# Optimization experiments

Measured on AMD Instinct MI355X. Metric: run time of the kernel, lower is better.

The kernel has to match this reference:

```python
import jax, jax.numpy as jnp
import numpy as np

P, F, V = 2048, 8192, 2048


def setup_inputs() -> dict:
    key = jax.random.key(0)
    k1, k2, k3 = jax.random.split(key, 3)
    points = jax.random.normal(k1, (P, 3), dtype=jnp.float32)
    vertices = jax.random.normal(k2, (V, 3), dtype=jnp.float32)
    faces = jax.random.randint(k3, (F, 3), 0, V, dtype=jnp.int32)
    return {"points": points, "vertices": vertices, "faces": faces}


def _triangle_weights(points, a, b, c):
    """Barycentric weights of closest point on each triangle (a,b,c) [F,3]
    for each point [P,3], via Ericson's region classification.
    All pairwise dot products expanded so only [P,F] scalars are materialized
    (never [P,F,3] differences)."""
    ab = b - a  # [F,3]
    ac = c - a  # [F,3]
    pab = points @ ab.T  # [P,F] = dot(p, ab)
    pac = points @ ac.T  # [P,F] = dot(p, ac)
    d1 = pab - jnp.sum(a * ab, -1)  # dot(ab, p-a)
    d2 = pac - jnp.sum(a * ac, -1)  # dot(ac, p-a)
    d3 = pab - jnp.sum(b * ab, -1)  # dot(ab, p-b)
    d4 = pac - jnp.sum(b * ac, -1)  # dot(ac, p-b)
    d5 = pab - jnp.sum(c * ab, -1)  # dot(ab, p-c)
    d6 = pac - jnp.sum(c * ac, -1)  # dot(ac, p-c)
    vc = d1 * d4 - d3 * d2
    vb = d5 * d2 - d1 * d6
    va = d3 * d6 - d5 * d4

    def sdiv(n, d):
        ds = jnp.where(d == 0, 1.0, d)
        return n / ds

    # region 7 (interior) is the default; overwrite with higher-priority
    denom = va + vb + vc
    v7 = sdiv(vb, denom)
    w7 = sdiv(vc, denom)
    w1, w2, w3 = 1.0 - v7 - w7, v7, w7
    # region 6: edge bc
    t6 = sdiv(d4 - d3, (d4 - d3) + (d5 - d6))
    m6 = (va <= 0) & (d4 - d3 >= 0) & (d5 - d6 >= 0)
    w1 = jnp.where(m6, 0.0, w1)
    w2 = jnp.where(m6, 1.0 - t6, w2)
    w3 = jnp.where(m6, t6, w3)
    # region 5: edge ac
    t5 = sdiv(d2, d2 - d6)
    m5 = (vb <= 0) & (d2 >= 0) & (d6 <= 0)
    w1 = jnp.where(m5, 1.0 - t5, w1)
    w2 = jnp.where(m5, 0.0, w2)
    w3 = jnp.where(m5, t5, w3)
    # region 4: vertex c
    m4 = (d6 >= 0) & (d5 <= d6)
    w1 = jnp.where(m4, 0.0, w1)
    w2 = jnp.where(m4, 0.0, w2)
    w3 = jnp.where(m4, 1.0, w3)
    # region 3: edge ab
    t3 = sdiv(d1, d1 - d3)
    m3 = (vc <= 0) & (d1 >= 0) & (d3 <= 0)
    w1 = jnp.where(m3, 1.0 - t3, w1)
    w2 = jnp.where(m3, t3, w2)
    w3 = jnp.where(m3, 0.0, w3)
    # region 2: vertex b
    m2 = (d3 >= 0) & (d4 <= d3)
    w1 = jnp.where(m2, 0.0, w1)
    w2 = jnp.where(m2, 1.0, w2)
    w3 = jnp.where(m2, 0.0, w3)
    # region 1: vertex a
    m1 = (d1 <= 0) & (d2 <= 0)
    w1 = jnp.where(m1, 1.0, w1)
    w2 = jnp.where(m1, 0.0, w2)
    w3 = jnp.where(m1, 0.0, w3)
    return w1, w2, w3  # each [P,F]


def reference(points, vertices, faces):
    # gather per-face vertex triples (the f1/f2/f3 of the torch module)
    a = vertices[faces[:, 0]]  # [F,3]
    b = vertices[faces[:, 1]]
    c = vertices[faces[:, 2]]
    w1, w2, w3 = _triangle_weights(points, a, b, c)  # [P,F] each
    cp = w1[..., None] * a + w2[..., None] * b + w3[..., None] * c  # [P,F,3]
    dist = jnp.sum((points[:, None, :] - cp) ** 2, axis=-1)  # [P,F]
    idx = jnp.argmin(dist, axis=1)  # [P] closest face per point
    gather = lambda w: jnp.take_along_axis(w, idx[:, None], axis=1)[:, 0]
    return idx, gather(w1), gather(w2), gather(w3)
```

## Files before the change

kernel.cpp:

```cpp
#include <hip/hip_runtime.h>
#include <cstdint>

#pragma clang fp contract(off)

typedef float v2f __attribute__((ext_vector_type(2)));

#define P_N 2048
#define F_N 8192
#define V_N 2048

#define TPB 256
#define FACES_PER_TILE 32

__device__ __forceinline__ void face_setup(
    const float* __restrict__ vertices, const int* __restrict__ faces, int f,
    float* fd)
{
#pragma clang fp contract(off)
    int i0 = faces[3 * f + 0];
    int i1 = faces[3 * f + 1];
    int i2 = faces[3 * f + 2];
    float ax = vertices[3 * i0 + 0], ay = vertices[3 * i0 + 1], az = vertices[3 * i0 + 2];
    float bx = vertices[3 * i1 + 0], by = vertices[3 * i1 + 1], bz = vertices[3 * i1 + 2];
    float cx = vertices[3 * i2 + 0], cy = vertices[3 * i2 + 1], cz = vertices[3 * i2 + 2];
    float abx = bx - ax, aby = by - ay, abz = bz - az;
    float acx = cx - ax, acy = cy - ay, acz = cz - az;
    float daab = (ax * abx + ay * aby) + az * abz;
    float daac = (ax * acx + ay * acy) + az * acz;
    float dbab = (bx * abx + by * aby) + bz * abz;
    float dbac = (bx * acx + by * acy) + bz * acz;
    float dcab = (cx * abx + cy * aby) + cz * abz;
    float dcac = (cx * acx + cy * acy) + cz * acz;
    fd[0] = ax;  fd[1] = ay;  fd[2] = az;
    fd[3] = bx;  fd[4] = by;  fd[5] = bz;
    fd[6] = cx;  fd[7] = cy;  fd[8] = cz;
    fd[9] = abx; fd[10] = aby; fd[11] = abz;
    fd[12] = acx; fd[13] = acy; fd[14] = acz;
    fd[15] = daab; fd[16] = daac; fd[17] = dbab;
    fd[18] = dbac; fd[19] = dcab; fd[20] = dcac;
}

__device__ __forceinline__ void region_w(
    float d1, float d2, float d3, float d4, float d5, float d6,
    float va, float vb, float vc, float e63, float e65, float denom,
    float& w1, float& w2, float& w3)
{
#pragma clang fp contract(off)
    bool m1 = (d1 <= 0.0f) & (d2 <= 0.0f);
    bool m2 = (d3 >= 0.0f) & (d4 <= d3);
    bool m3 = (vc <= 0.0f) & (d1 >= 0.0f) & (d3 <= 0.0f);
    bool m4 = (d6 >= 0.0f) & (d5 <= d6);
    bool m5 = (vb <= 0.0f) & (d2 >= 0.0f) & (d6 <= 0.0f);
    bool m6 = (va <= 0.0f) & (e63 >= 0.0f) & (e65 >= 0.0f);
    bool anym = m1 | m2 | m3 | m4 | m5 | m6;

    float n1  = m1 ? 0.0f : m2 ? 0.0f : m3 ? d1          : m4 ? 0.0f : m5 ? d2          : m6 ? e63         : vb;
    float ds1 = m1 ? 1.0f : m2 ? 1.0f : m3 ? (d1 - d3)   : m4 ? 1.0f : m5 ? (d2 - d6)   : m6 ? (e63 + e65) : denom;
    ds1 = (ds1 == 0.0f) ? 1.0f : ds1;
    float n2  = anym ? 0.0f : vc;
    float ds2 = anym ? 1.0f : ((denom == 0.0f) ? 1.0f : denom);

    float q1 = n1 / ds1;
    float q2 = n2 / ds2;
    float u = (1.0f - q1) - q2;

    w1 = m1 ? 1.0f : m2 ? 0.0f : m3 ? u    : m4 ? 0.0f : m5 ? u    : m6 ? 0.0f : u;
    w2 = m1 ? 0.0f : m2 ? 1.0f : m3 ? q1   : m4 ? 0.0f : m5 ? 0.0f : m6 ? u    : q1;
    w3 = m1 ? 0.0f : m2 ? 0.0f : m3 ? 0.0f : m4 ? 1.0f : m5 ? q1   : m6 ? q1   : q2;
}

__device__ __forceinline__ void tri_eval_exact(
    float px, float py, float pz,
    const float* fd,
    float& w1o, float& w2o, float& w3o, float& disto)
{
#pragma clang fp contract(off)
    const float ax = fd[0], ay = fd[1], az = fd[2];
    const float bx = fd[3], by = fd[4], bz = fd[5];
    const float cx = fd[6], cy = fd[7], cz = fd[8];
    const float abx = fd[9], aby = fd[10], abz = fd[11];
    const float acx = fd[12], acy = fd[13], acz = fd[14];
    const float daab = fd[15], daac = fd[16], dbab = fd[17];
    const float dbac = fd[18], dcab = fd[19], dcac = fd[20];

    float pab = fmaf(pz, abz, fmaf(py, aby, px * abx));
    float pac = fmaf(pz, acz, fmaf(py, acy, px * acx));

    float d1 = pab - daab;
    float d2 = pac - daac;
    float d3 = pab - dbab;
    float d4 = pac - dbac;
    float d5 = pab - dcab;
    float d6 = pac - dcac;

    float vc = d1 * d4 - d3 * d2;
    float vb = d5 * d2 - d1 * d6;
    float va = d3 * d6 - d5 * d4;

    float denom = (va + vb) + vc;
    float dn = (denom == 0.0f) ? 1.0f : denom;
    float v7 = vb / dn;
    float w7 = vc / dn;
    float w1 = (1.0f - v7) - w7;
    float w2 = v7;
    float w3 = w7;

    float e63 = d4 - d3;
    float e65 = d5 - d6;
    float t6d = e63 + e65; t6d = (t6d == 0.0f) ? 1.0f : t6d;
    float t6 = e63 / t6d;
    if ((va <= 0.0f) & (e63 >= 0.0f) & (e65 >= 0.0f)) { w1 = 0.0f; w2 = 1.0f - t6; w3 = t6; }

    float t5d = d2 - d6; t5d = (t5d == 0.0f) ? 1.0f : t5d;
    float t5 = d2 / t5d;
    if ((vb <= 0.0f) & (d2 >= 0.0f) & (d6 <= 0.0f)) { w1 = 1.0f - t5; w2 = 0.0f; w3 = t5; }

    if ((d6 >= 0.0f) & (d5 <= d6)) { w1 = 0.0f; w2 = 0.0f; w3 = 1.0f; }

    float t3d = d1 - d3; t3d = (t3d == 0.0f) ? 1.0f : t3d;
    float t3 = d1 / t3d;
    if ((vc <= 0.0f) & (d1 >= 0.0f) & (d3 <= 0.0f)) { w1 = 1.0f - t3; w2 = t3; w3 = 0.0f; }

    if ((d3 >= 0.0f) & (d4 <= d3)) { w1 = 0.0f; w2 = 1.0f; w3 = 0.0f; }

    if ((d1 <= 0.0f) & (d2 <= 0.0f)) { w1 = 1.0f; w2 = 0.0f; w3 = 0.0f; }

    float cpx = (w1 * ax + w2 * bx) + w3 * cx;
    float cpy = (w1 * ay + w2 * by) + w3 * cy;
    float cpz = (w1 * az + w2 * bz) + w3 * cz;
    float dx = px - cpx, dy = py - cpy, dz = pz - cpz;
    float dist = (dx * dx + dy * dy) + dz * dz;

    w1o = w1; w2o = w2; w3o = w3; disto = dist;
}

__global__ __launch_bounds__(TPB) void k_scan(
    const float* __restrict__ points,
    const float* __restrict__ vertices,
    const int* __restrict__ faces,
    unsigned long long* __restrict__ best)
{
#pragma clang fp contract(off)
    __shared__ float sq[21][FACES_PER_TILE];

    const int pblk = blockIdx.x;
    const int fblk = blockIdx.y;
    const int t = threadIdx.x;

    if (t < FACES_PER_TILE) {
        int f = fblk * FACES_PER_TILE + t;
        float fd[21];
        face_setup(vertices, faces, f, fd);
#pragma unroll
        for (int k = 0; k < 21; ++k) sq[k][t] = fd[k];
    }
    __syncthreads();

    const int p = pblk * TPB + t;
    const float px = points[3 * p + 0];
    const float py = points[3 * p + 1];
    const float pz = points[3 * p + 2];
    const v2f pxv = {px, px};
    const v2f pyv = {py, py};
    const v2f pzv = {pz, pz};

    unsigned int bestdb = 0xffffffffu;
    int bestf = 0;
    const int fbase = fblk * FACES_PER_TILE;

#pragma unroll 2
    for (int j = 0; j < FACES_PER_TILE; j += 2) {
#define LD2(q) (*(const v2f*)&sq[q][j])
        v2f axv = LD2(0),  ayv = LD2(1),  azv = LD2(2);
        v2f bxv = LD2(3),  byv = LD2(4),  bzv = LD2(5);
        v2f cxv = LD2(6),  cyv = LD2(7),  czv = LD2(8);
        v2f abxv = LD2(9),  abyv = LD2(10), abzv = LD2(11);
        v2f acxv = LD2(12), acyv = LD2(13), aczv = LD2(14);
        v2f daabv = LD2(15), daacv = LD2(16), dbabv = LD2(17);
        v2f dbacv = LD2(18), dcabv = LD2(19), dcacv = LD2(20);
#undef LD2

        v2f pab = __builtin_elementwise_fma(pzv, abzv,
                    __builtin_elementwise_fma(pyv, abyv, pxv * abxv));
        v2f pac = __builtin_elementwise_fma(pzv, aczv,
                    __builtin_elementwise_fma(pyv, acyv, pxv * acxv));

        v2f d1 = pab - daabv;
        v2f d2 = pac - daacv;
        v2f d3 = pab - dbabv;
        v2f d4 = pac - dbacv;
        v2f d5 = pab - dcabv;
        v2f d6 = pac - dcacv;

        v2f vcv = d1 * d4 - d3 * d2;
        v2f vbv = d5 * d2 - d1 * d6;
        v2f vav = d3 * d6 - d5 * d4;

        v2f e63 = d4 - d3;
        v2f e65 = d5 - d6;
        v2f denom = (vav + vbv) + vcv;

        float w1a, w2a, w3a, w1b, w2b, w3b;
        region_w(d1.x, d2.x, d3.x, d4.x, d5.x, d6.x,
                 vav.x, vbv.x, vcv.x, e63.x, e65.x, denom.x, w1a, w2a, w3a);
        region_w(d1.y, d2.y, d3.y, d4.y, d5.y, d6.y,
                 vav.y, vbv.y, vcv.y, e63.y, e65.y, denom.y, w1b, w2b, w3b);

        v2f w1v = {w1a, w1b};
        v2f w2v = {w2a, w2b};
        v2f w3v = {w3a, w3b};

        v2f cpx = (w1v * axv + w2v * bxv) + w3v * cxv;
        v2f cpy = (w1v * ayv + w2v * byv) + w3v * cyv;
        v2f cpz = (w1v * azv + w2v * bzv) + w3v * czv;
        v2f dx = pxv - cpx, dy = pyv - cpy, dz = pzv - cpz;
        v2f dist = (dx * dx + dy * dy) + dz * dz;

        float da = dist.x;
        float db = dist.y;
        unsigned int ua = __float_as_uint(da);
        unsigned int ub = __float_as_uint(db);
        if (da != da) ua = 0u;
        if (db != db) ub = 0u;
        if (ua < bestdb) { bestdb = ua; bestf = fbase + j; }
        if (ub < bestdb) { bestdb = ub; bestf = fbase + j + 1; }
    }

    unsigned long long key =
        ((unsigned long long)bestdb << 32) | (unsigned int)bestf;
    atomicMin(&best[p], key);
}

__global__ __launch_bounds__(TPB) void k_final(
    const float* __restrict__ points,
    const float* __restrict__ vertices,
    const int* __restrict__ faces,
    const unsigned long long* __restrict__ best,
    float* __restrict__ out)
{
    const int p = blockIdx.x * TPB + threadIdx.x;
    if (p >= P_N) return;
    unsigned long long bk = best[p];
    int f = (int)(bk & 0xffffffffull);

    float fd[21];
    face_setup(vertices, faces, f, fd);

    const float px = points[3 * p + 0];
    const float py = points[3 * p + 1];
    const float pz = points[3 * p + 2];
    float w1, w2, w3, dist;
    tri_eval_exact(px, py, pz, fd, w1, w2, w3, dist);

    out[p] = (float)f;
    out[P_N + p] = w1;
    out[2 * P_N + p] = w2;
    out[3 * P_N + p] = w3;
}

extern "C" void kernel_launch(void* const* d_in, const int* in_sizes, int n_in,
                              void* d_out, int out_size, void* d_ws, size_t ws_size,
                              hipStream_t stream)
{
    const float* points = (const float*)d_in[0];
    const float* vertices = (const float*)d_in[1];
    const int* faces = (const int*)d_in[2];
    float* out = (float*)d_out;
    unsigned long long* best = (unsigned long long*)d_ws;

    hipMemsetAsync(d_ws, 0xFF, P_N * sizeof(unsigned long long), stream);

    dim3 grid(P_N / TPB, F_N / FACES_PER_TILE);
    k_scan<<<grid, TPB, 0, stream>>>(points, vertices, faces, best);
    k_final<<<(P_N + TPB - 1) / TPB, TPB, 0, stream>>>(points, vertices, faces, best, out);
}
```

Baseline: 55.95 us.

## Add bound-screening pass so exact evaluation runs only for candidate faces

Splits the brute-force scan into two passes. A screening kernel computes cheap per-face lower and upper distance bounds for each point, stores 16-bit truncated lower bounds in a workspace buffer and atomically reduces the minimum upper bound. An exact kernel then runs the full triangle evaluation only for faces whose lower bound does not exceed that minimum. The aim is to skip most exact evaluations, at the cost of an extra launch, a large lower-bound buffer (about 32 MB written and reread), divergent branches, and reliance on hand-tuned numeric margins for correctness. If the workspace is too small it falls back to the old full scan.

```diff
diff --git a/kernel.cpp b/kernel.cpp
--- a/kernel.cpp
+++ b/kernel.cpp
@@ -7,10 +7,15 @@
 
 #define P_N 2048
 #define F_N 8192
-#define V_N 2048
-
 #define TPB 256
-#define FACES_PER_TILE 32
+#define FPT 32
+#define NT (F_N / FPT)
+
+#define WS_BEST_OFF   0
+#define WS_MINUB_OFF  16384
+#define WS_LB_OFF     24576
+#define WS_NEEDED     (24576ull + (unsigned long long)(F_N / 2) * P_N * 4ull)
+
 
 __device__ __forceinline__ void face_setup(
     const float* __restrict__ vertices, const int* __restrict__ faces, int f,
@@ -40,6 +45,307 @@
     fd[18] = dbac; fd[19] = dcab; fd[20] = dcac;
 }
 
+__device__ __forceinline__ void tri_eval_exact(
+    float px, float py, float pz,
+    const float* fd,
+    float& w1o, float& w2o, float& w3o, float& disto)
+{
+#pragma clang fp contract(off)
+    const float ax = fd[0], ay = fd[1], az = fd[2];
+    const float bx = fd[3], by = fd[4], bz = fd[5];
+    const float cx = fd[6], cy = fd[7], cz = fd[8];
+    const float abx = fd[9], aby = fd[10], abz = fd[11];
+    const float acx = fd[12], acy = fd[13], acz = fd[14];
+    const float daab = fd[15], daac = fd[16], dbab = fd[17];
+    const float dbac = fd[18], dcab = fd[19], dcac = fd[20];
+
+    float pab = fmaf(pz, abz, fmaf(py, aby, px * abx));
+    float pac = fmaf(pz, acz, fmaf(py, acy, px * acx));
+
+    float d1 = pab - daab;
+    float d2 = pac - daac;
+    float d3 = pab - dbab;
+    float d4 = pac - dbac;
+    float d5 = pab - dcab;
+    float d6 = pac - dcac;
+
+    float vc = d1 * d4 - d3 * d2;
+    float vb = d5 * d2 - d1 * d6;
+    float va = d3 * d6 - d5 * d4;
+
+    float denom = (va + vb) + vc;
+    float dn = (denom == 0.0f) ? 1.0f : denom;
+    float v7 = vb / dn;
+    float w7 = vc / dn;
+    float w1 = (1.0f - v7) - w7;
+    float w2 = v7;
+    float w3 = w7;
+
+    float e63 = d4 - d3;
+    float e65 = d5 - d6;
+    float t6d = e63 + e65; t6d = (t6d == 0.0f) ? 1.0f : t6d;
+    float t6 = e63 / t6d;
+    if ((va <= 0.0f) & (e63 >= 0.0f) & (e65 >= 0.0f)) { w1 = 0.0f; w2 = 1.0f - t6; w3 = t6; }
+
+    float t5d = d2 - d6; t5d = (t5d == 0.0f) ? 1.0f : t5d;
+    float t5 = d2 / t5d;
+    if ((vb <= 0.0f) & (d2 >= 0.0f) & (d6 <= 0.0f)) { w1 = 1.0f - t5; w2 = 0.0f; w3 = t5; }
+
+    if ((d6 >= 0.0f) & (d5 <= d6)) { w1 = 0.0f; w2 = 0.0f; w3 = 1.0f; }
+
+    float t3d = d1 - d3; t3d = (t3d == 0.0f) ? 1.0f : t3d;
+    float t3 = d1 / t3d;
+    if ((vc <= 0.0f) & (d1 >= 0.0f) & (d3 <= 0.0f)) { w1 = 1.0f - t3; w2 = t3; w3 = 0.0f; }
+
+    if ((d3 >= 0.0f) & (d4 <= d3)) { w1 = 0.0f; w2 = 1.0f; w3 = 0.0f; }
+
+    if ((d1 <= 0.0f) & (d2 <= 0.0f)) { w1 = 1.0f; w2 = 0.0f; w3 = 0.0f; }
+
+    float cpx = (w1 * ax + w2 * bx) + w3 * cx;
+    float cpy = (w1 * ay + w2 * by) + w3 * cy;
+    float cpz = (w1 * az + w2 * bz) + w3 * cz;
+    float dx = px - cpx, dy = py - cpy, dz = pz - cpz;
+    float dist = (dx * dx + dy * dy) + dz * dz;
+
+    w1o = w1; w2o = w2; w3o = w3; disto = dist;
+}
+
+
+#define NARR 35
+enum {
+    iAX = 0, iAY, iAZ,
+    iABX, iABY, iABZ,
+    iACX, iACY, iACZ,
+    iA, iB, iC, iD, iE, iF,
+    iKCS, iKCT, iKCC,
+    iKBS, iKBT, iKBC,
+    iKAS, iKAT, iKAC,
+    iNX, iNY, iNZ, iMND,
+    iIAB, iIAC, iIBC, iINN,
+    iABAB, iACAC,
+    iMARG
+};
+
+__device__ __forceinline__ void stage_screen(
+    const float* __restrict__ v, const int* __restrict__ fc, int f, int slot,
+    float sq[NARR][FPT])
+{
+#pragma clang fp contract(off)
+    int i0 = fc[3 * f + 0], i1 = fc[3 * f + 1], i2 = fc[3 * f + 2];
+    float ax = v[3 * i0], ay = v[3 * i0 + 1], az = v[3 * i0 + 2];
+    float bx = v[3 * i1], by = v[3 * i1 + 1], bz = v[3 * i1 + 2];
+    float cx = v[3 * i2], cy = v[3 * i2 + 1], cz = v[3 * i2 + 2];
+    float abx = bx - ax, aby = by - ay, abz = bz - az;
+    float acx = cx - ax, acy = cy - ay, acz = cz - az;
+    float A = (ax * abx + ay * aby) + az * abz;
+    float B = (ax * acx + ay * acy) + az * acz;
+    float C = (bx * abx + by * aby) + bz * abz;
+    float D = (bx * acx + by * acy) + bz * acz;
+    float E = (cx * abx + cy * aby) + cz * abz;
+    float F = (cx * acx + cy * acy) + cz * acz;
+    float kcs = B - D, kct = C - A, kcc = A * D - C * B;
+    float kbs = F - B, kbt = A - E, kbc = E * B - A * F;
+    float kas = D - F, kat = E - C, kac = C * F - E * D;
+    float nx = aby * acz - abz * acy;
+    float ny = abz * acx - abx * acz;
+    float nz = abx * acy - aby * acx;
+    float nn = (nx * nx + ny * ny) + nz * nz;
+    float abab = (abx * abx + aby * aby) + abz * abz;
+    float acac = (acx * acx + acy * acy) + acz * acz;
+    float bcx = cx - bx, bcy = cy - by, bcz = cz - bz;
+    float bcbc = (bcx * bcx + bcy * bcy) + bcz * bcz;
+    float inv_ab = abab > 0.0f ? 1.0f / abab : 0.0f;
+    float inv_ac = acac > 0.0f ? 1.0f / acac : 0.0f;
+    float inv_bc = bcbc > 0.0f ? 1.0f / bcbc : 0.0f;
+    float inv_nn = nn >= 1e-2f ? 1.0f / nn : 0.0f;
+    float L2 = abab + acac;
+    float infl = 1e-4f * L2 * sqrtf(L2) * inv_nn;
+    float marg = 3e-4f + infl * infl;
+    bool bad = (nn < 1e-2f) | (abab < 1e-3f) | (acac < 1e-3f) | (bcbc < 1e-3f) | (marg > 0.25f);
+    if (bad) marg = 1e30f;
+    float mnda = -((nx * ax + ny * ay) + nz * az);
+
+    sq[iAX][slot] = ax;  sq[iAY][slot] = ay;  sq[iAZ][slot] = az;
+    sq[iABX][slot] = abx; sq[iABY][slot] = aby; sq[iABZ][slot] = abz;
+    sq[iACX][slot] = acx; sq[iACY][slot] = acy; sq[iACZ][slot] = acz;
+    sq[iA][slot] = A; sq[iB][slot] = B; sq[iC][slot] = C;
+    sq[iD][slot] = D; sq[iE][slot] = E; sq[iF][slot] = F;
+    sq[iKCS][slot] = kcs; sq[iKCT][slot] = kct; sq[iKCC][slot] = kcc;
+    sq[iKBS][slot] = kbs; sq[iKBT][slot] = kbt; sq[iKBC][slot] = kbc;
+    sq[iKAS][slot] = kas; sq[iKAT][slot] = kat; sq[iKAC][slot] = kac;
+    sq[iNX][slot] = nx; sq[iNY][slot] = ny; sq[iNZ][slot] = nz; sq[iMND][slot] = mnda;
+    sq[iIAB][slot] = inv_ab; sq[iIAC][slot] = inv_ac; sq[iIBC][slot] = inv_bc; sq[iINN][slot] = inv_nn;
+    sq[iABAB][slot] = abab; sq[iACAC][slot] = acac;
+    sq[iMARG][slot] = marg;
+}
+
+__device__ __forceinline__ void screen_face(
+    float d1, float d2, float d3, float d4, float d5, float d6,
+    float va, float vb, float vc, float e63, float e65,
+    float pa2, float pb2, float pc2,
+    float sub3, float sub5, float sub6, float subI,
+    float marg,
+    float& ubmin, unsigned& lb16)
+{
+    bool m1 = (d1 <= 0.0f) & (d2 <= 0.0f);
+    bool m2 = (d3 >= 0.0f) & (d4 <= d3);
+    bool m3 = (vc <= 0.0f) & (d1 >= 0.0f) & (d3 <= 0.0f);
+    bool m4 = (d6 >= 0.0f) & (d5 <= d6);
+    bool m5 = (vb <= 0.0f) & (d2 >= 0.0f) & (d6 <= 0.0f);
+    bool m6 = (va <= 0.0f) & (e63 >= 0.0f) & (e65 >= 0.0f);
+    float screen = m1 ? pa2 : m2 ? pb2 : m3 ? sub3 : m4 ? pc2 : m5 ? sub5 : m6 ? sub6 : subI;
+    screen = fmaxf(screen, 0.0f);
+    bool bad = marg > 0.25f;
+    float ub = bad ? (pa2 + 3e-4f) : (screen + marg);
+    ubmin = fminf(ubmin, ub);
+    float lb = fmaxf(fmaf(0.99f, screen, -marg), 0.0f);
+    lb16 = __float_as_uint(lb) >> 16;
+}
+
+__global__ __launch_bounds__(TPB) void k_screen(
+    const float* __restrict__ points,
+    const float* __restrict__ vertices,
+    const int* __restrict__ faces,
+    unsigned* __restrict__ minub,
+    unsigned* __restrict__ lbout)
+{
+#pragma clang fp contract(off)
+    __shared__ float sq[NARR][FPT];
+
+    const int pblk = blockIdx.x;
+    const int fblk = blockIdx.y;
+    const int t = threadIdx.x;
+
+    if (t < FPT) stage_screen(vertices, faces, fblk * FPT + t, t, sq);
+    __syncthreads();
+
+    const int p = pblk * TPB + t;
+    const float px = points[3 * p + 0];
+    const float py = points[3 * p + 1];
+    const float pz = points[3 * p + 2];
+    const v2f pxv = {px, px}, pyv = {py, py}, pzv = {pz, pz};
+    const v2f n2v = {-2.0f, -2.0f};
+
+    float ubmin = 3e38f;
+
+#pragma unroll 2
+    for (int jp = 0; jp < FPT / 2; ++jp) {
+        const int j = jp * 2;
+#define L2D(k) (*(const v2f*)&sq[k][j])
+        v2f s = __builtin_elementwise_fma(pzv, L2D(iABZ),
+                    __builtin_elementwise_fma(pyv, L2D(iABY), pxv * L2D(iABX)));
+        v2f tt = __builtin_elementwise_fma(pzv, L2D(iACZ),
+                    __builtin_elementwise_fma(pyv, L2D(iACY), pxv * L2D(iACX)));
+
+        v2f d1 = s - L2D(iA);
+        v2f d2 = tt - L2D(iB);
+        v2f d3 = s - L2D(iC);
+        v2f d4 = tt - L2D(iD);
+        v2f d5 = s - L2D(iE);
+        v2f d6 = tt - L2D(iF);
+
+        v2f vc = __builtin_elementwise_fma(s, L2D(iKCS),
+                    __builtin_elementwise_fma(tt, L2D(iKCT), L2D(iKCC)));
+        v2f vb = __builtin_elementwise_fma(s, L2D(iKBS),
+                    __builtin_elementwise_fma(tt, L2D(iKBT), L2D(iKBC)));
+        v2f va = __builtin_elementwise_fma(s, L2D(iKAS),
+                    __builtin_elementwise_fma(tt, L2D(iKAT), L2D(iKAC)));
+
+        v2f e63 = d4 - d3;
+        v2f e65 = d5 - d6;
+
+        v2f nd = __builtin_elementwise_fma(L2D(iNZ), pzv,
+                    __builtin_elementwise_fma(L2D(iNY), pyv,
+                        __builtin_elementwise_fma(L2D(iNX), pxv, L2D(iMND))));
+
+        v2f dax = pxv - L2D(iAX);
+        v2f day = pyv - L2D(iAY);
+        v2f daz = pzv - L2D(iAZ);
+        v2f pa2 = __builtin_elementwise_fma(daz, daz,
+                     __builtin_elementwise_fma(day, day, dax * dax));
+        v2f pb2 = __builtin_elementwise_fma(n2v, d1, pa2) + L2D(iABAB);
+        v2f pc2 = __builtin_elementwise_fma(n2v, d2, pa2) + L2D(iACAC);
+
+        v2f sub3 = __builtin_elementwise_fma(-(d1 * L2D(iIAB)), d1, pa2);
+        v2f sub5 = __builtin_elementwise_fma(-(d2 * L2D(iIAC)), d2, pa2);
+        v2f sub6 = __builtin_elementwise_fma(-(e63 * L2D(iIBC)), e63, pb2);
+        v2f subI = (nd * L2D(iINN)) * nd;
+
+        v2f mg = L2D(iMARG);
+#undef L2D
+
+        unsigned lo16, hi16;
+        screen_face(d1.x, d2.x, d3.x, d4.x, d5.x, d6.x, va.x, vb.x, vc.x,
+                    e63.x, e65.x, pa2.x, pb2.x, pc2.x,
+                    sub3.x, sub5.x, sub6.x, subI.x, mg.x, ubmin, lo16);
+        screen_face(d1.y, d2.y, d3.y, d4.y, d5.y, d6.y, va.y, vb.y, vc.y,
+                    e63.y, e65.y, pa2.y, pb2.y, pc2.y,
+                    sub3.y, sub5.y, sub6.y, subI.y, mg.y, ubmin, hi16);
+
+        lbout[(fblk * (FPT / 2) + jp) * P_N + p] = lo16 | (hi16 << 16);
+    }
+
+    atomicMin(&minub[p], __float_as_uint(ubmin));
+}
+
+
+__global__ __launch_bounds__(TPB) void k_exact(
+    const float* __restrict__ points,
+    const float* __restrict__ vertices,
+    const int* __restrict__ faces,
+    const unsigned* __restrict__ minub,
+    const unsigned* __restrict__ lbin,
+    unsigned long long* __restrict__ best)
+{
+    __shared__ float sf[FPT][21];
+
+    const int pblk = blockIdx.x;
+    const int fblk = blockIdx.y;
+    const int t = threadIdx.x;
+
+    if (t < FPT) {
+        float fd[21];
+        face_setup(vertices, faces, fblk * FPT + t, fd);
+#pragma unroll
+        for (int k = 0; k < 21; ++k) sf[t][k] = fd[k];
+    }
+    __syncthreads();
+
+    const int p = pblk * TPB + t;
+    const float px = points[3 * p + 0];
+    const float py = points[3 * p + 1];
+    const float pz = points[3 * p + 2];
+    const float mub = __uint_as_float(minub[p]);
+
+    unsigned long long bk = ~0ull;
+    const int fbase = fblk * FPT;
+
+    for (int jp = 0; jp < FPT / 2; ++jp) {
+        unsigned w = lbin[(fblk * (FPT / 2) + jp) * P_N + p];
+        float lo = __uint_as_float(w << 16);
+        float hi = __uint_as_float(w & 0xFFFF0000u);
+        if (lo <= mub) {
+            float w1, w2, w3, dist;
+            tri_eval_exact(px, py, pz, &sf[jp * 2][0], w1, w2, w3, dist);
+            unsigned db = __float_as_uint(dist);
+            if (dist != dist) db = 0u;
+            unsigned long long key = ((unsigned long long)db << 32) | (unsigned)(fbase + jp * 2);
+            bk = (key < bk) ? key : bk;
+        }
+        if (hi <= mub) {
+            float w1, w2, w3, dist;
+            tri_eval_exact(px, py, pz, &sf[jp * 2 + 1][0], w1, w2, w3, dist);
+            unsigned db = __float_as_uint(dist);
+            if (dist != dist) db = 0u;
+            unsigned long long key = ((unsigned long long)db << 32) | (unsigned)(fbase + jp * 2 + 1);
+            bk = (key < bk) ? key : bk;
+        }
+    }
+
+    if (bk != ~0ull) atomicMin(&best[p], bk);
+}
+
+
 __device__ __forceinline__ void region_w(
     float d1, float d2, float d3, float d4, float d5, float d6,
     float va, float vb, float vc, float e63, float e65, float denom,
@@ -54,8 +360,8 @@
     bool m6 = (va <= 0.0f) & (e63 >= 0.0f) & (e65 >= 0.0f);
     bool anym = m1 | m2 | m3 | m4 | m5 | m6;
 
-    float n1  = m1 ? 0.0f : m2 ? 0.0f : m3 ? d1          : m4 ? 0.0f : m5 ? d2          : m6 ? e63         : vb;
-    float ds1 = m1 ? 1.0f : m2 ? 1.0f : m3 ? (d1 - d3)   : m4 ? 1.0f : m5 ? (d2 - d6)   : m6 ? (e63 + e65) : denom;
+    float n1  = m1 ? 0.0f : m2 ? 0.0f : m3 ? d1        : m4 ? 0.0f : m5 ? d2        : m6 ? e63       : vb;
+    float ds1 = m1 ? 1.0f : m2 ? 1.0f : m3 ? (d1 - d3) : m4 ? 1.0f : m5 ? (d2 - d6) : m6 ? (e63 + e65) : denom;
     ds1 = (ds1 == 0.0f) ? 1.0f : ds1;
     float n2  = anym ? 0.0f : vc;
     float ds2 = anym ? 1.0f : ((denom == 0.0f) ? 1.0f : denom);
@@ -69,86 +375,21 @@
     w3 = m1 ? 0.0f : m2 ? 0.0f : m3 ? 0.0f : m4 ? 1.0f : m5 ? q1   : m6 ? q1   : q2;
 }
 
-__device__ __forceinline__ void tri_eval_exact(
-    float px, float py, float pz,
-    const float* fd,
-    float& w1o, float& w2o, float& w3o, float& disto)
-{
-#pragma clang fp contract(off)
-    const float ax = fd[0], ay = fd[1], az = fd[2];
-    const float bx = fd[3], by = fd[4], bz = fd[5];
-    const float cx = fd[6], cy = fd[7], cz = fd[8];
-    const float abx = fd[9], aby = fd[10], abz = fd[11];
-    const float acx = fd[12], acy = fd[13], acz = fd[14];
-    const float daab = fd[15], daac = fd[16], dbab = fd[17];
-    const float dbac = fd[18], dcab = fd[19], dcac = fd[20];
-
-    float pab = fmaf(pz, abz, fmaf(py, aby, px * abx));
-    float pac = fmaf(pz, acz, fmaf(py, acy, px * acx));
-
-    float d1 = pab - daab;
-    float d2 = pac - daac;
-    float d3 = pab - dbab;
-    float d4 = pac - dbac;
-    float d5 = pab - dcab;
-    float d6 = pac - dcac;
-
-    float vc = d1 * d4 - d3 * d2;
-    float vb = d5 * d2 - d1 * d6;
-    float va = d3 * d6 - d5 * d4;
-
-    float denom = (va + vb) + vc;
-    float dn = (denom == 0.0f) ? 1.0f : denom;
-    float v7 = vb / dn;
-    float w7 = vc / dn;
-    float w1 = (1.0f - v7) - w7;
-    float w2 = v7;
-    float w3 = w7;
-
-    float e63 = d4 - d3;
-    float e65 = d5 - d6;
-    float t6d = e63 + e65; t6d = (t6d == 0.0f) ? 1.0f : t6d;
-    float t6 = e63 / t6d;
-    if ((va <= 0.0f) & (e63 >= 0.0f) & (e65 >= 0.0f)) { w1 = 0.0f; w2 = 1.0f - t6; w3 = t6; }
-
-    float t5d = d2 - d6; t5d = (t5d == 0.0f) ? 1.0f : t5d;
-    float t5 = d2 / t5d;
-    if ((vb <= 0.0f) & (d2 >= 0.0f) & (d6 <= 0.0f)) { w1 = 1.0f - t5; w2 = 0.0f; w3 = t5; }
-
-    if ((d6 >= 0.0f) & (d5 <= d6)) { w1 = 0.0f; w2 = 0.0f; w3 = 1.0f; }
-
-    float t3d = d1 - d3; t3d = (t3d == 0.0f) ? 1.0f : t3d;
-    float t3 = d1 / t3d;
-    if ((vc <= 0.0f) & (d1 >= 0.0f) & (d3 <= 0.0f)) { w1 = 1.0f - t3; w2 = t3; w3 = 0.0f; }
-
-    if ((d3 >= 0.0f) & (d4 <= d3)) { w1 = 0.0f; w2 = 1.0f; w3 = 0.0f; }
-
-    if ((d1 <= 0.0f) & (d2 <= 0.0f)) { w1 = 1.0f; w2 = 0.0f; w3 = 0.0f; }
-
-    float cpx = (w1 * ax + w2 * bx) + w3 * cx;
-    float cpy = (w1 * ay + w2 * by) + w3 * cy;
-    float cpz = (w1 * az + w2 * bz) + w3 * cz;
-    float dx = px - cpx, dy = py - cpy, dz = pz - cpz;
-    float dist = (dx * dx + dy * dy) + dz * dz;
-
-    w1o = w1; w2o = w2; w3o = w3; disto = dist;
-}
-
-__global__ __launch_bounds__(TPB) void k_scan(
+__global__ __launch_bounds__(TPB) void k_scan_full(
     const float* __restrict__ points,
     const float* __restrict__ vertices,
     const int* __restrict__ faces,
     unsigned long long* __restrict__ best)
 {
 #pragma clang fp contract(off)
-    __shared__ float sq[21][FACES_PER_TILE];
+    __shared__ float sq[21][FPT];
 
     const int pblk = blockIdx.x;
     const int fblk = blockIdx.y;
     const int t = threadIdx.x;
 
-    if (t < FACES_PER_TILE) {
-        int f = fblk * FACES_PER_TILE + t;
+    if (t < FPT) {
+        int f = fblk * FPT + t;
         float fd[21];
         face_setup(vertices, faces, f, fd);
 #pragma unroll
@@ -160,16 +401,14 @@
     const float px = points[3 * p + 0];
     const float py = points[3 * p + 1];
     const float pz = points[3 * p + 2];
-    const v2f pxv = {px, px};
-    const v2f pyv = {py, py};
-    const v2f pzv = {pz, pz};
+    const v2f pxv = {px, px}, pyv = {py, py}, pzv = {pz, pz};
 
     unsigned int bestdb = 0xffffffffu;
     int bestf = 0;
-    const int fbase = fblk * FACES_PER_TILE;
+    const int fbase = fblk * FPT;
 
 #pragma unroll 2
-    for (int j = 0; j < FACES_PER_TILE; j += 2) {
+    for (int j = 0; j < FPT; j += 2) {
 #define LD2(q) (*(const v2f*)&sq[q][j])
         v2f axv = LD2(0),  ayv = LD2(1),  azv = LD2(2);
         v2f bxv = LD2(3),  byv = LD2(4),  bzv = LD2(5);
@@ -231,6 +470,7 @@
     atomicMin(&best[p], key);
 }
 
+
 __global__ __launch_bounds__(TPB) void k_final(
     const float* __restrict__ points,
     const float* __restrict__ vertices,
@@ -266,11 +506,23 @@
     const float* vertices = (const float*)d_in[1];
     const int* faces = (const int*)d_in[2];
     float* out = (float*)d_out;
-    unsigned long long* best = (unsigned long long*)d_ws;
-
-    hipMemsetAsync(d_ws, 0xFF, P_N * sizeof(unsigned long long), stream);
-
-    dim3 grid(P_N / TPB, F_N / FACES_PER_TILE);
-    k_scan<<<grid, TPB, 0, stream>>>(points, vertices, faces, best);
+
+    char* ws = (char*)d_ws;
+    unsigned long long* best = (unsigned long long*)(ws + WS_BEST_OFF);
+
+    hipMemsetAsync(best, 0xFF, P_N * sizeof(unsigned long long), stream);
+
+    dim3 grid(P_N / TPB, NT);
+
+    if (ws_size >= WS_NEEDED) {
+        unsigned* minub = (unsigned*)(ws + WS_MINUB_OFF);
+        unsigned* lbbuf = (unsigned*)(ws + WS_LB_OFF);
+        hipMemsetAsync(minub, 0x7F, P_N * sizeof(unsigned), stream);
+        k_screen<<<grid, TPB, 0, stream>>>(points, vertices, faces, minub, lbbuf);
+        k_exact<<<grid, TPB, 0, stream>>>(points, vertices, faces, minub, lbbuf, best);
+    } else {
+        k_scan_full<<<grid, TPB, 0, stream>>>(points, vertices, faces, best);
+    }
+
     k_final<<<(P_N + TPB - 1) / TPB, TPB, 0, stream>>>(points, vertices, faces, best, out);
 }
```

New measurement: 70.59 us. +26.2%, slower.

## Add screen-then-verify path with per-face lower bounds and candidate queue

Applied to the files above, without the earlier changes.

Adds a three-kernel path: precompute an extended per-face table, run a cheap branch-light screening pass that yields 8-bit quantized lower bounds plus a per-point upper bound, then evaluate the exact Ericson routine only on faces whose bound passes the threshold. The screening pass avoids the per-face divisions of the exact scan. In exchange it writes a 16 MB byte-code array to workspace and reads it back. The margins are heuristic, so correctness depends on them, and if the workspace is too small the code falls back to the old path.

```diff
diff --git a/kernel.cpp b/kernel.cpp
--- a/kernel.cpp
+++ b/kernel.cpp
@@ -7,10 +7,17 @@
 
 #define P_N 2048
 #define F_N 8192
-#define V_N 2048
-
 #define TPB 256
-#define FACES_PER_TILE 32
+#define FPT 32
+#define NT (F_N / FPT)
+#define NC 44
+#define QCAP 192
+
+#define WS_TAB_OFF    0
+#define WS_MINUB_OFF  1441792
+#define WS_LB_OFF     2097152
+#define WS_NEEDED     (WS_LB_OFF + (size_t)P_N * F_N)
+
 
 __device__ __forceinline__ void face_setup(
     const float* __restrict__ vertices, const int* __restrict__ faces, int f,
@@ -40,6 +47,317 @@
     fd[18] = dbac; fd[19] = dcab; fd[20] = dcac;
 }
 
+__device__ __forceinline__ void tri_eval_exact(
+    float px, float py, float pz,
+    const float* fd,
+    float& w1o, float& w2o, float& w3o, float& disto)
+{
+#pragma clang fp contract(off)
+    const float ax = fd[0], ay = fd[1], az = fd[2];
+    const float bx = fd[3], by = fd[4], bz = fd[5];
+    const float cx = fd[6], cy = fd[7], cz = fd[8];
+    const float abx = fd[9], aby = fd[10], abz = fd[11];
+    const float acx = fd[12], acy = fd[13], acz = fd[14];
+    const float daab = fd[15], daac = fd[16], dbab = fd[17];
+    const float dbac = fd[18], dcab = fd[19], dcac = fd[20];
+
+    float pab = fmaf(pz, abz, fmaf(py, aby, px * abx));
+    float pac = fmaf(pz, acz, fmaf(py, acy, px * acx));
+
+    float d1 = pab - daab;
+    float d2 = pac - daac;
+    float d3 = pab - dbab;
+    float d4 = pac - dbac;
+    float d5 = pab - dcab;
+    float d6 = pac - dcac;
+
+    float vc = d1 * d4 - d3 * d2;
+    float vb = d5 * d2 - d1 * d6;
+    float va = d3 * d6 - d5 * d4;
+
+    float denom = (va + vb) + vc;
+    float dn = (denom == 0.0f) ? 1.0f : denom;
+    float v7 = vb / dn;
+    float w7 = vc / dn;
+    float w1 = (1.0f - v7) - w7;
+    float w2 = v7;
+    float w3 = w7;
+
+    float e63 = d4 - d3;
+    float e65 = d5 - d6;
+    float t6d = e63 + e65; t6d = (t6d == 0.0f) ? 1.0f : t6d;
+    float t6 = e63 / t6d;
+    if ((va <= 0.0f) & (e63 >= 0.0f) & (e65 >= 0.0f)) { w1 = 0.0f; w2 = 1.0f - t6; w3 = t6; }
+
+    float t5d = d2 - d6; t5d = (t5d == 0.0f) ? 1.0f : t5d;
+    float t5 = d2 / t5d;
+    if ((vb <= 0.0f) & (d2 >= 0.0f) & (d6 <= 0.0f)) { w1 = 1.0f - t5; w2 = 0.0f; w3 = t5; }
+
+    if ((d6 >= 0.0f) & (d5 <= d6)) { w1 = 0.0f; w2 = 0.0f; w3 = 1.0f; }
+
+    float t3d = d1 - d3; t3d = (t3d == 0.0f) ? 1.0f : t3d;
+    float t3 = d1 / t3d;
+    if ((vc <= 0.0f) & (d1 >= 0.0f) & (d3 <= 0.0f)) { w1 = 1.0f - t3; w2 = t3; w3 = 0.0f; }
+
+    if ((d3 >= 0.0f) & (d4 <= d3)) { w1 = 0.0f; w2 = 1.0f; w3 = 0.0f; }
+
+    if ((d1 <= 0.0f) & (d2 <= 0.0f)) { w1 = 1.0f; w2 = 0.0f; w3 = 0.0f; }
+
+    float cpx = (w1 * ax + w2 * bx) + w3 * cx;
+    float cpy = (w1 * ay + w2 * by) + w3 * cy;
+    float cpz = (w1 * az + w2 * bz) + w3 * cz;
+    float dx = px - cpx, dy = py - cpy, dz = pz - cpz;
+    float dist = (dx * dx + dy * dy) + dz * dz;
+
+    w1o = w1; w2o = w2; w3o = w3; disto = dist;
+}
+
+
+__global__ __launch_bounds__(64) void k_prep(
+    const float* __restrict__ vertices, const int* __restrict__ faces,
+    float* __restrict__ tab, unsigned* __restrict__ minub)
+{
+#pragma clang fp contract(off)
+    int f = blockIdx.x * 64 + threadIdx.x;
+    if (f < F_N) {
+        float td[NC];
+        face_setup(vertices, faces, f, td);
+        float ax = td[0], ay = td[1], az = td[2];
+        float bx = td[3], by = td[4], bz = td[5];
+        float cx = td[6], cy = td[7], cz = td[8];
+        float abx = td[9], aby = td[10], abz = td[11];
+        float acx = td[12], acy = td[13], acz = td[14];
+        float A = td[15], B = td[16], C = td[17], D = td[18], E = td[19], F = td[20];
+        td[21] = B - D; td[22] = C - A; td[23] = A * D - C * B;
+        td[24] = F - B; td[25] = A - E; td[26] = E * B - A * F;
+        td[27] = D - F; td[28] = E - C; td[29] = C * F - E * D;
+        float nx = aby * acz - abz * acy;
+        float ny = abz * acx - abx * acz;
+        float nz = abx * acy - aby * acx;
+        float nn = (nx * nx + ny * ny) + nz * nz;
+        float abab = (abx * abx + aby * aby) + abz * abz;
+        float acac = (acx * acx + acy * acy) + acz * acz;
+        float bcx = cx - bx, bcy = cy - by, bcz = cz - bz;
+        float bcbc = (bcx * bcx + bcy * bcy) + bcz * bcz;
+        float inv_ab = abab > 0.0f ? 1.0f / abab : 0.0f;
+        float inv_ac = acac > 0.0f ? 1.0f / acac : 0.0f;
+        float inv_bc = bcbc > 0.0f ? 1.0f / bcbc : 0.0f;
+        float inv_nn = nn >= 1e-2f ? 1.0f / nn : 0.0f;
+        float L2 = abab + acac;
+        float infl = 1e-4f * L2 * sqrtf(L2) * inv_nn;
+        float marg = 3e-4f + infl * infl;
+        bool bad = (nn < 1e-2f) | (abab < 1e-3f) | (acac < 1e-3f) | (bcbc < 1e-3f) | (marg > 0.25f);
+        if (bad) marg = 1e30f;
+        td[30] = nx; td[31] = ny; td[32] = nz;
+        td[33] = -((nx * ax + ny * ay) + nz * az);
+        td[34] = inv_ab; td[35] = inv_ac; td[36] = inv_bc; td[37] = inv_nn;
+        td[38] = abab; td[39] = acac; td[40] = marg;
+        td[41] = 0.0f; td[42] = 0.0f; td[43] = 0.0f;
+#pragma unroll
+        for (int k = 0; k < NC; k += 4)
+            *(float4*)&tab[f * NC + k] = *(float4*)&td[k];
+    }
+    if (f < P_N) minub[f] = 0x7f7f7f7fu;
+}
+
+
+__device__ __forceinline__ void screen_face2(
+    float d1, float d2, float d3, float d4, float d5, float d6,
+    float va, float vb, float vc, float e63, float e65,
+    float pa2, float pb2, float pc2,
+    float sub3, float sub5, float sub6, float subI,
+    float marg,
+    float& ubmin, int& codeout)
+{
+    bool m1 = (d1 <= 0.0f) & (d2 <= 0.0f);
+    bool m2 = (d3 >= 0.0f) & (d4 <= d3);
+    bool m3 = (vc <= 0.0f) & (d1 >= 0.0f) & (d3 <= 0.0f);
+    bool m4 = (d6 >= 0.0f) & (d5 <= d6);
+    bool m5 = (vb <= 0.0f) & (d2 >= 0.0f) & (d6 <= 0.0f);
+    bool m6 = (va <= 0.0f) & (e63 >= 0.0f) & (e65 >= 0.0f);
+    float screen = m1 ? pa2 : m2 ? pb2 : m3 ? sub3 : m4 ? pc2 : m5 ? sub5 : m6 ? sub6 : subI;
+    screen = fmaxf(screen, 0.0f);
+    bool bad = marg > 0.25f;
+    if (!bad) ubmin = fminf(ubmin, screen + marg);
+    float lb = bad ? 0.0f : fmaxf(fmaf(0.99f, screen, -marg), 0.0f);
+    int code = (int)(__float_as_uint(lb) >> 20) - 896;
+    codeout = code < 0 ? 0 : (code > 255 ? 255 : code);
+}
+
+__global__ __launch_bounds__(TPB) void k_screen(
+    const float* __restrict__ points,
+    const float* __restrict__ tab,
+    unsigned* __restrict__ minub,
+    unsigned* __restrict__ lbw)
+{
+#pragma clang fp contract(off)
+    __shared__ float sq[NC][FPT];
+
+    const int pblk = blockIdx.x, fblk = blockIdx.y, t = threadIdx.x;
+    const int fbase = fblk * FPT;
+    {
+        int q0 = t >> 5, slot = t & 31;
+        for (int qq = q0; qq < NC; qq += 8)
+            sq[qq][slot] = tab[(fbase + slot) * NC + qq];
+    }
+    __syncthreads();
+
+    const int p = pblk * TPB + t;
+    const float px = points[3 * p + 0];
+    const float py = points[3 * p + 1];
+    const float pz = points[3 * p + 2];
+    const v2f pxv = {px, px}, pyv = {py, py}, pzv = {pz, pz};
+    const v2f n2v = {-2.0f, -2.0f};
+
+    float ubmin = 3e38f;
+    unsigned cw[FPT / 4];
+#pragma unroll
+    for (int k = 0; k < FPT / 4; ++k) cw[k] = 0;
+
+#pragma unroll 2
+    for (int jp = 0; jp < FPT / 2; ++jp) {
+        const int j = jp * 2;
+#define L2D(k) (*(const v2f*)&sq[k][j])
+        v2f s = __builtin_elementwise_fma(pzv, L2D(11),
+                    __builtin_elementwise_fma(pyv, L2D(10), pxv * L2D(9)));
+        v2f tt = __builtin_elementwise_fma(pzv, L2D(14),
+                    __builtin_elementwise_fma(pyv, L2D(13), pxv * L2D(12)));
+
+        v2f d1 = s - L2D(15);
+        v2f d2 = tt - L2D(16);
+        v2f d3 = s - L2D(17);
+        v2f d4 = tt - L2D(18);
+        v2f d5 = s - L2D(19);
+        v2f d6 = tt - L2D(20);
+
+        v2f vc = __builtin_elementwise_fma(s, L2D(21),
+                    __builtin_elementwise_fma(tt, L2D(22), L2D(23)));
+        v2f vb = __builtin_elementwise_fma(s, L2D(24),
+                    __builtin_elementwise_fma(tt, L2D(25), L2D(26)));
+        v2f va = __builtin_elementwise_fma(s, L2D(27),
+                    __builtin_elementwise_fma(tt, L2D(28), L2D(29)));
+
+        v2f e63 = d4 - d3;
+        v2f e65 = d5 - d6;
+
+        v2f nd = __builtin_elementwise_fma(L2D(32), pzv,
+                    __builtin_elementwise_fma(L2D(31), pyv,
+                        __builtin_elementwise_fma(L2D(30), pxv, L2D(33))));
+
+        v2f dax = pxv - L2D(0);
+        v2f day = pyv - L2D(1);
+        v2f daz = pzv - L2D(2);
+        v2f pa2 = __builtin_elementwise_fma(daz, daz,
+                     __builtin_elementwise_fma(day, day, dax * dax));
+        v2f pb2 = __builtin_elementwise_fma(n2v, d1, pa2) + L2D(38);
+        v2f pc2 = __builtin_elementwise_fma(n2v, d2, pa2) + L2D(39);
+
+        v2f sub3 = __builtin_elementwise_fma(-(d1 * L2D(34)), d1, pa2);
+        v2f sub5 = __builtin_elementwise_fma(-(d2 * L2D(35)), d2, pa2);
+        v2f sub6 = __builtin_elementwise_fma(-(e63 * L2D(36)), e63, pb2);
+        v2f subI = (nd * L2D(37)) * nd;
+
+        v2f mg = L2D(40);
+#undef L2D
+
+        int c0, c1;
+        screen_face2(d1.x, d2.x, d3.x, d4.x, d5.x, d6.x, va.x, vb.x, vc.x,
+                     e63.x, e65.x, pa2.x, pb2.x, pc2.x,
+                     sub3.x, sub5.x, sub6.x, subI.x, mg.x, ubmin, c0);
+        screen_face2(d1.y, d2.y, d3.y, d4.y, d5.y, d6.y, va.y, vb.y, vc.y,
+                     e63.y, e65.y, pa2.y, pb2.y, pc2.y,
+                     sub3.y, sub5.y, sub6.y, subI.y, mg.y, ubmin, c1);
+
+        cw[jp >> 1] |= ((unsigned)c0 << (8 * ((2 * jp) & 3)))
+                     | ((unsigned)c1 << (8 * ((2 * jp + 1) & 3)));
+    }
+
+    atomicMin(&minub[p], __float_as_uint(ubmin));
+
+    unsigned* dst = &lbw[p * (F_N / 4) + fblk * (FPT / 4)];
+    *(uint4*)&dst[0] = make_uint4(cw[0], cw[1], cw[2], cw[3]);
+    *(uint4*)&dst[4] = make_uint4(cw[4], cw[5], cw[6], cw[7]);
+}
+
+
+__global__ __launch_bounds__(TPB) void k_exact(
+    const float* __restrict__ points,
+    const float* __restrict__ tab,
+    const unsigned* __restrict__ minub,
+    const unsigned* __restrict__ lbw,
+    float* __restrict__ out)
+{
+    __shared__ unsigned short qbuf[4][QCAP];
+    __shared__ int qcnt[4];
+
+    const int w = threadIdx.x >> 6;
+    const int lane = threadIdx.x & 63;
+    const int p = blockIdx.x * 4 + w;
+
+    if (lane == 0) qcnt[w] = 0;
+    __syncthreads();
+
+    const float px = points[3 * p + 0];
+    const float py = points[3 * p + 1];
+    const float pz = points[3 * p + 2];
+    int thr = (int)(minub[p] >> 20) - 896;
+    thr = thr < 0 ? 0 : (thr > 255 ? 255 : thr);
+
+    const unsigned* mylb = &lbw[p * (F_N / 4)];
+    for (int it = 0; it < F_N / 256; ++it) {
+        unsigned word = mylb[it * 64 + lane];
+#pragma unroll
+        for (int b = 0; b < 4; ++b) {
+            int code = (word >> (8 * b)) & 255;
+            if (code <= thr) {
+                int slot = atomicAdd(&qcnt[w], 1);
+                if (slot < QCAP) qbuf[w][slot] = (unsigned short)((it * 64 + lane) * 4 + b);
+            }
+        }
+    }
+    __syncthreads();
+    const int n = qcnt[w];
+
+    unsigned long long bestk = ~0ull;
+    float bw1 = 0.0f, bw2 = 0.0f, bw3 = 0.0f;
+
+    auto eval1 = [&](int f) {
+        float fdl[21];
+#pragma unroll
+        for (int k = 0; k < 20; k += 4)
+            *(float4*)&fdl[k] = *(const float4*)&tab[f * NC + k];
+        fdl[20] = tab[f * NC + 20];
+        float w1, w2, w3, dist;
+        tri_eval_exact(px, py, pz, fdl, w1, w2, w3, dist);
+        unsigned db = __float_as_uint(dist);
+        if (dist != dist) db = 0u;
+        unsigned long long key = ((unsigned long long)db << 32) | (unsigned)f;
+        if (key < bestk) { bestk = key; bw1 = w1; bw2 = w2; bw3 = w3; }
+    };
+
+    if (n > QCAP) {
+        for (int f = lane; f < F_N; f += 64) eval1(f);
+    } else {
+        for (int r = lane; r < n; r += 64) eval1((int)qbuf[w][r]);
+    }
+
+    const unsigned long long myk = bestk;
+    unsigned long long red = bestk;
+#pragma unroll
+    for (int off = 32; off > 0; off >>= 1) {
+        unsigned long long o = __shfl_xor(red, off, 64);
+        red = o < red ? o : red;
+    }
+    if (myk == red) {
+        int f = (int)(red & 0xffffffffull);
+        out[p] = (float)f;
+        out[P_N + p] = bw1;
+        out[2 * P_N + p] = bw2;
+        out[3 * P_N + p] = bw3;
+    }
+}
+
+
 __device__ __forceinline__ void region_w(
     float d1, float d2, float d3, float d4, float d5, float d6,
     float va, float vb, float vc, float e63, float e65, float denom,
@@ -54,8 +372,8 @@
     bool m6 = (va <= 0.0f) & (e63 >= 0.0f) & (e65 >= 0.0f);
     bool anym = m1 | m2 | m3 | m4 | m5 | m6;
 
-    float n1  = m1 ? 0.0f : m2 ? 0.0f : m3 ? d1          : m4 ? 0.0f : m5 ? d2          : m6 ? e63         : vb;
-    float ds1 = m1 ? 1.0f : m2 ? 1.0f : m3 ? (d1 - d3)   : m4 ? 1.0f : m5 ? (d2 - d6)   : m6 ? (e63 + e65) : denom;
+    float n1  = m1 ? 0.0f : m2 ? 0.0f : m3 ? d1        : m4 ? 0.0f : m5 ? d2        : m6 ? e63         : vb;
+    float ds1 = m1 ? 1.0f : m2 ? 1.0f : m3 ? (d1 - d3) : m4 ? 1.0f : m5 ? (d2 - d6) : m6 ? (e63 + e65) : denom;
     ds1 = (ds1 == 0.0f) ? 1.0f : ds1;
     float n2  = anym ? 0.0f : vc;
     float ds2 = anym ? 1.0f : ((denom == 0.0f) ? 1.0f : denom);
@@ -69,107 +387,33 @@
     w3 = m1 ? 0.0f : m2 ? 0.0f : m3 ? 0.0f : m4 ? 1.0f : m5 ? q1   : m6 ? q1   : q2;
 }
 
-__device__ __forceinline__ void tri_eval_exact(
-    float px, float py, float pz,
-    const float* fd,
-    float& w1o, float& w2o, float& w3o, float& disto)
-{
-#pragma clang fp contract(off)
-    const float ax = fd[0], ay = fd[1], az = fd[2];
-    const float bx = fd[3], by = fd[4], bz = fd[5];
-    const float cx = fd[6], cy = fd[7], cz = fd[8];
-    const float abx = fd[9], aby = fd[10], abz = fd[11];
-    const float acx = fd[12], acy = fd[13], acz = fd[14];
-    const float daab = fd[15], daac = fd[16], dbab = fd[17];
-    const float dbac = fd[18], dcab = fd[19], dcac = fd[20];
-
-    float pab = fmaf(pz, abz, fmaf(py, aby, px * abx));
-    float pac = fmaf(pz, acz, fmaf(py, acy, px * acx));
-
-    float d1 = pab - daab;
-    float d2 = pac - daac;
-    float d3 = pab - dbab;
-    float d4 = pac - dbac;
-    float d5 = pab - dcab;
-    float d6 = pac - dcac;
-
-    float vc = d1 * d4 - d3 * d2;
-    float vb = d5 * d2 - d1 * d6;
-    float va = d3 * d6 - d5 * d4;
-
-    float denom = (va + vb) + vc;
-    float dn = (denom == 0.0f) ? 1.0f : denom;
-    float v7 = vb / dn;
-    float w7 = vc / dn;
-    float w1 = (1.0f - v7) - w7;
-    float w2 = v7;
-    float w3 = w7;
-
-    float e63 = d4 - d3;
-    float e65 = d5 - d6;
-    float t6d = e63 + e65; t6d = (t6d == 0.0f) ? 1.0f : t6d;
-    float t6 = e63 / t6d;
-    if ((va <= 0.0f) & (e63 >= 0.0f) & (e65 >= 0.0f)) { w1 = 0.0f; w2 = 1.0f - t6; w3 = t6; }
-
-    float t5d = d2 - d6; t5d = (t5d == 0.0f) ? 1.0f : t5d;
-    float t5 = d2 / t5d;
-    if ((vb <= 0.0f) & (d2 >= 0.0f) & (d6 <= 0.0f)) { w1 = 1.0f - t5; w2 = 0.0f; w3 = t5; }
-
-    if ((d6 >= 0.0f) & (d5 <= d6)) { w1 = 0.0f; w2 = 0.0f; w3 = 1.0f; }
-
-    float t3d = d1 - d3; t3d = (t3d == 0.0f) ? 1.0f : t3d;
-    float t3 = d1 / t3d;
-    if ((vc <= 0.0f) & (d1 >= 0.0f) & (d3 <= 0.0f)) { w1 = 1.0f - t3; w2 = t3; w3 = 0.0f; }
-
-    if ((d3 >= 0.0f) & (d4 <= d3)) { w1 = 0.0f; w2 = 1.0f; w3 = 0.0f; }
-
-    if ((d1 <= 0.0f) & (d2 <= 0.0f)) { w1 = 1.0f; w2 = 0.0f; w3 = 0.0f; }
-
-    float cpx = (w1 * ax + w2 * bx) + w3 * cx;
-    float cpy = (w1 * ay + w2 * by) + w3 * cy;
-    float cpz = (w1 * az + w2 * bz) + w3 * cz;
-    float dx = px - cpx, dy = py - cpy, dz = pz - cpz;
-    float dist = (dx * dx + dy * dy) + dz * dz;
-
-    w1o = w1; w2o = w2; w3o = w3; disto = dist;
-}
-
-__global__ __launch_bounds__(TPB) void k_scan(
+__global__ __launch_bounds__(TPB) void k_scan_full(
     const float* __restrict__ points,
     const float* __restrict__ vertices,
     const int* __restrict__ faces,
     unsigned long long* __restrict__ best)
 {
 #pragma clang fp contract(off)
-    __shared__ float sq[21][FACES_PER_TILE];
-
-    const int pblk = blockIdx.x;
-    const int fblk = blockIdx.y;
-    const int t = threadIdx.x;
-
-    if (t < FACES_PER_TILE) {
-        int f = fblk * FACES_PER_TILE + t;
+    __shared__ float sq[21][FPT];
+    const int pblk = blockIdx.x, fblk = blockIdx.y, t = threadIdx.x;
+    if (t < FPT) {
         float fd[21];
-        face_setup(vertices, faces, f, fd);
+        face_setup(vertices, faces, fblk * FPT + t, fd);
 #pragma unroll
         for (int k = 0; k < 21; ++k) sq[k][t] = fd[k];
     }
     __syncthreads();
 
     const int p = pblk * TPB + t;
-    const float px = points[3 * p + 0];
-    const float py = points[3 * p + 1];
-    const float pz = points[3 * p + 2];
-    const v2f pxv = {px, px};
-    const v2f pyv = {py, py};
-    const v2f pzv = {pz, pz};
+    const float px = points[3 * p], py = points[3 * p + 1], pz = points[3 * p + 2];
+    const v2f pxv = {px, px}, pyv = {py, py}, pzv = {pz, pz};
 
     unsigned int bestdb = 0xffffffffu;
     int bestf = 0;
-    const int fbase = fblk * FACES_PER_TILE;
+    const int fbase = fblk * FPT;
 
 #pragma unroll 2
-    for (int j = 0; j < FACES_PER_TILE; j += 2) {
+    for (int j = 0; j < FPT; j += 2) {
 #define LD2(q) (*(const v2f*)&sq[q][j])
         v2f axv = LD2(0),  ayv = LD2(1),  azv = LD2(2);
         v2f bxv = LD2(3),  byv = LD2(4),  bzv = LD2(5);
@@ -179,25 +423,16 @@
         v2f daabv = LD2(15), daacv = LD2(16), dbabv = LD2(17);
         v2f dbacv = LD2(18), dcabv = LD2(19), dcacv = LD2(20);
 #undef LD2
-
         v2f pab = __builtin_elementwise_fma(pzv, abzv,
                     __builtin_elementwise_fma(pyv, abyv, pxv * abxv));
         v2f pac = __builtin_elementwise_fma(pzv, aczv,
                     __builtin_elementwise_fma(pyv, acyv, pxv * acxv));
-
-        v2f d1 = pab - daabv;
-        v2f d2 = pac - daacv;
-        v2f d3 = pab - dbabv;
-        v2f d4 = pac - dbacv;
-        v2f d5 = pab - dcabv;
-        v2f d6 = pac - dcacv;
-
+        v2f d1 = pab - daabv, d2 = pac - daacv, d3 = pab - dbabv;
+        v2f d4 = pac - dbacv, d5 = pab - dcabv, d6 = pac - dcacv;
         v2f vcv = d1 * d4 - d3 * d2;
         v2f vbv = d5 * d2 - d1 * d6;
         v2f vav = d3 * d6 - d5 * d4;
-
-        v2f e63 = d4 - d3;
-        v2f e65 = d5 - d6;
+        v2f e63 = d4 - d3, e65 = d5 - d6;
         v2f denom = (vav + vbv) + vcv;
 
         float w1a, w2a, w3a, w1b, w2b, w3b;
@@ -206,20 +441,15 @@
         region_w(d1.y, d2.y, d3.y, d4.y, d5.y, d6.y,
                  vav.y, vbv.y, vcv.y, e63.y, e65.y, denom.y, w1b, w2b, w3b);
 
-        v2f w1v = {w1a, w1b};
-        v2f w2v = {w2a, w2b};
-        v2f w3v = {w3a, w3b};
-
+        v2f w1v = {w1a, w1b}, w2v = {w2a, w2b}, w3v = {w3a, w3b};
         v2f cpx = (w1v * axv + w2v * bxv) + w3v * cxv;
         v2f cpy = (w1v * ayv + w2v * byv) + w3v * cyv;
         v2f cpz = (w1v * azv + w2v * bzv) + w3v * czv;
         v2f dx = pxv - cpx, dy = pyv - cpy, dz = pzv - cpz;
         v2f dist = (dx * dx + dy * dy) + dz * dz;
 
-        float da = dist.x;
-        float db = dist.y;
-        unsigned int ua = __float_as_uint(da);
-        unsigned int ub = __float_as_uint(db);
+        float da = dist.x, db = dist.y;
+        unsigned ua = __float_as_uint(da), ub = __float_as_uint(db);
         if (da != da) ua = 0u;
         if (db != db) ub = 0u;
         if (ua < bestdb) { bestdb = ua; bestf = fbase + j; }
@@ -240,18 +470,11 @@
 {
     const int p = blockIdx.x * TPB + threadIdx.x;
     if (p >= P_N) return;
-    unsigned long long bk = best[p];
-    int f = (int)(bk & 0xffffffffull);
-
+    int f = (int)(best[p] & 0xffffffffull);
     float fd[21];
     face_setup(vertices, faces, f, fd);
-
-    const float px = points[3 * p + 0];
-    const float py = points[3 * p + 1];
-    const float pz = points[3 * p + 2];
     float w1, w2, w3, dist;
-    tri_eval_exact(px, py, pz, fd, w1, w2, w3, dist);
-
+    tri_eval_exact(points[3 * p], points[3 * p + 1], points[3 * p + 2], fd, w1, w2, w3, dist);
     out[p] = (float)f;
     out[P_N + p] = w1;
     out[2 * P_N + p] = w2;
@@ -266,11 +489,20 @@
     const float* vertices = (const float*)d_in[1];
     const int* faces = (const int*)d_in[2];
     float* out = (float*)d_out;
-    unsigned long long* best = (unsigned long long*)d_ws;
-
-    hipMemsetAsync(d_ws, 0xFF, P_N * sizeof(unsigned long long), stream);
-
-    dim3 grid(P_N / TPB, F_N / FACES_PER_TILE);
-    k_scan<<<grid, TPB, 0, stream>>>(points, vertices, faces, best);
-    k_final<<<(P_N + TPB - 1) / TPB, TPB, 0, stream>>>(points, vertices, faces, best, out);
-}
+    char* ws = (char*)d_ws;
+
+    if (ws_size >= WS_NEEDED) {
+        float* tab = (float*)(ws + WS_TAB_OFF);
+        unsigned* minub = (unsigned*)(ws + WS_MINUB_OFF);
+        unsigned* lbw = (unsigned*)(ws + WS_LB_OFF);
+
+        k_prep<<<F_N / 64, 64, 0, stream>>>(vertices, faces, tab, minub);
+        k_screen<<<dim3(P_N / TPB, NT), TPB, 0, stream>>>(points, tab, minub, lbw);
+        k_exact<<<P_N / 4, TPB, 0, stream>>>(points, tab, minub, lbw, out);
+    } else {
+        unsigned long long* best = (unsigned long long*)ws;
+        hipMemsetAsync(best, 0xFF, P_N * sizeof(unsigned long long), stream);
+        k_scan_full<<<dim3(P_N / TPB, NT), TPB, 0, stream>>>(points, vertices, faces, best);
+        k_final<<<(P_N + TPB - 1) / TPB, TPB, 0, stream>>>(points, vertices, faces, best, out);
+    }
+}
```

After: 75.96 us. 35.8% more time.
